# Kernel optimization log

Hardware: AMD Instinct MI355X
Metric: run time of the kernel (lower is better)

The kernel has to match this reference:

```python
import jax, jax.numpy as jnp
import numpy as np

NEG_MASK = -999.0  # matches masked_fill_(-999) in the torch source

def setup_inputs() -> dict:
    key = jax.random.key(0)
    ks = jax.random.split(key, 8)
    B, N, D = 4, 2048, 768      # batch, nodes, in_dim
    H, Do = 6, 128              # att_head, out_dim (D == H*Do)
    feat_in = jax.random.normal(ks[0], (B, N, D), dtype=jnp.float32)
    adj = jax.random.randint(ks[1], (B, N, N), 0, 2).astype(jnp.int32)
    W = jax.random.normal(ks[2], (H, D, Do), dtype=jnp.float32) * (1.0 / np.sqrt(D))
    b = jnp.zeros((Do,), dtype=jnp.float32)
    w_src = jax.random.normal(ks[3], (H, Do, 1), dtype=jnp.float32) * (1.0 / np.sqrt(Do))
    w_dst = jax.random.normal(ks[4], (H, Do, 1), dtype=jnp.float32) * (1.0 / np.sqrt(Do))
    H_w = jax.random.normal(ks[5], (D, D), dtype=jnp.float32) * (1.0 / np.sqrt(D))
    H_b = jnp.zeros((D,), dtype=jnp.float32)
    return {"feat_in": feat_in, "adj": adj, "W": W, "b": b,
            "w_src": w_src, "w_dst": w_dst, "H_w": H_w, "H_b": H_b}

def reference(feat_in, adj, W, b, w_src, w_dst, H_w, H_b):
    leaky_alpha = 0.2
    B, N, D = feat_in.shape
    Hh = W.shape[0]
    # per-head projection: [B, H, N, Do]
    h = jnp.einsum('bni,hio->bhno', feat_in, W)
    th = jnp.tanh(h)
    attn_src = jnp.einsum('bhno,hoz->bhnz', th, w_src)  # [B,H,N,1]
    attn_dst = jnp.einsum('bhno,hoz->bhnz', th, w_dst)  # [B,H,N,1]
    # additive scores: src_i + dst_j -> [B,H,N,N]
    attn = attn_src + jnp.swapaxes(attn_dst, -1, -2)
    attn = jnp.where(attn >= 0, attn, leaky_alpha * attn)
    mask = (adj == 0)[:, None, :, :]  # [B,1,N,N]
    attn = jnp.where(mask, NEG_MASK, attn)
    attn = jax.nn.softmax(attn, axis=-1)
    feat_out = jnp.einsum('bhnm,bhmo->bhno', attn, h) + b  # [B,H,N,Do]
    feat_out = jnp.swapaxes(feat_out, 1, 2).reshape(B, N, -1)  # [B,N,H*Do]
    feat_out = jax.nn.elu(feat_out)
    gate = jax.nn.sigmoid(feat_in @ H_w.T + H_b)
    out = gate * feat_out + (1.0 - gate) * feat_in
    return out
```

## Files before the change

### kernel.cpp

```cpp
#include <hip/hip_runtime.h>
#include <hip/hip_bf16.h>

#define B_ 4
#define N_ 2048
#define D_ 768
#define H_ 6
#define Do_ 128
#define M_ (B_*N_)
#define C2_ (2*D_)
#define SROW 49152

typedef __attribute__((ext_vector_type(8))) short bf16x8;
typedef __attribute__((ext_vector_type(4))) float f32x4;
typedef __attribute__((ext_vector_type(4))) int int4v;
typedef __attribute__((ext_vector_type(2))) int int2v;
typedef __attribute__((ext_vector_type(4))) float float4v;
typedef __attribute__((ext_vector_type(4))) unsigned short ushort4v;

__device__ __forceinline__ float b2f(short s){
    unsigned u = ((unsigned)(unsigned short)s) << 16;
    return __builtin_bit_cast(float, u);
}
__device__ __forceinline__ short f2b(float f){
    unsigned u = __builtin_bit_cast(unsigned, f);
    unsigned r = (u + 0x7fffu + ((u >> 16) & 1u)) >> 16;
    return (short)r;
}
__device__ __forceinline__ int pk2(float a, float b){
    unsigned ua = __builtin_bit_cast(unsigned, a) + 0x8000u;
    unsigned ub = __builtin_bit_cast(unsigned, b) + 0x8000u;
    return (int)__builtin_amdgcn_perm(ub, ua, 0x07060302u);
}
__device__ __forceinline__ float fast_tanh(float x){
    float a = fabsf(x);
    float e = __expf(-2.0f * a);
    float t = (1.0f - e) / (1.0f + e);
    return copysignf(t, x);
}

#define HT_IDX(bh, n, o) ((((size_t)((bh)*64 + ((n) >> 5))*128 + (o))*32) + ((n) & 31))

__global__ __launch_bounds__(256) void k_prep_pack(const float* __restrict__ W,
                                                   const float* __restrict__ Hw,
                                                   const int* __restrict__ adj,
                                                   short* __restrict__ bmat,
                                                   unsigned char* __restrict__ pk){
    int bid = blockIdx.x, t = threadIdx.x;
    if (bid < C2_){
        int c = bid;
        if (c < D_){
            int hd = c >> 7, o = c & 127;
            const float* wp = W + hd*D_*Do_ + o;
            for (int k = t; k < D_; k += 256) bmat[c*D_ + k] = f2b(wp[k*Do_]);
        } else {
            int d = c - D_;
            const float* hp = Hw + d*D_;
            for (int k = t; k < D_; k += 256) bmat[c*D_ + k] = f2b(hp[k]);
        }
    } else {
        int g = (bid - C2_)*256 + t;
        const int* ap = adj + (size_t)g*8;
        int4v a0 = *(const int4v*)ap;
        int4v a1 = *(const int4v*)(ap + 4);
        unsigned by = 0;
        #pragma unroll
        for (int i = 0; i < 4; i++){
            by |= (a0[i] ? 1u : 0u) << i;
            by |= (a1[i] ? 1u : 0u) << (i + 4);
        }
        pk[g] = (unsigned char)by;
    }
}

__global__ __launch_bounds__(256) void k_gemm(const float* __restrict__ A,
                                              const short* __restrict__ Bm,
                                              short* __restrict__ ht,
                                              float* outg){
    __shared__ short As[128][72];
    __shared__ short Bs[128][72];
    int tid = threadIdx.x;
    int mBase = blockIdx.y * 128, cBase = blockIdx.x * 128;
    int wave = tid >> 6, lane = tid & 63, q = lane >> 4, nL = lane & 15;
    int wr = (wave >> 1) * 64, wc = (wave & 1) * 64;
    f32x4 acc[4][4] = {};
    for (int kk = 0; kk < D_; kk += 64){
        __syncthreads();
        #pragma unroll
        for (int i = 0; i < 8; i++){
            int idx = tid + i*256;
            int row = idx >> 4, c4 = (idx & 15) * 4;
            float4v av = *(const float4v*)&A[(mBase+row)*D_ + kk + c4];
            int2v w; w[0] = pk2(av[0], av[1]); w[1] = pk2(av[2], av[3]);
            *(int2v*)&As[row][c4] = w;
        }
        #pragma unroll
        for (int i = 0; i < 4; i++){
            int idx = tid + i*256;
            int row = idx >> 3, cs = (idx & 7) * 8;
            *(int4v*)&Bs[row][cs] = *(const int4v*)&Bm[(cBase+row)*D_ + kk + cs];
        }
        __syncthreads();
        #pragma unroll
        for (int k2 = 0; k2 < 64; k2 += 32){
            bf16x8 aF[4], bF[4];
            #pragma unroll
            for (int rt = 0; rt < 4; rt++) aF[rt] = *(const bf16x8*)&As[wr + rt*16 + nL][k2 + q*8];
            #pragma unroll
            for (int ct = 0; ct < 4; ct++) bF[ct] = *(const bf16x8*)&Bs[wc + ct*16 + nL][k2 + q*8];
            #pragma unroll
            for (int rt = 0; rt < 4; rt++)
                #pragma unroll
                for (int ct = 0; ct < 4; ct++)
                    acc[rt][ct] = __builtin_amdgcn_mfma_f32_16x16x32_bf16(aF[rt], bF[ct], acc[rt][ct], 0, 0, 0);
        }
    }
    if (cBase < D_){
        int hd = cBase >> 7;
        #pragma unroll
        for (int rt = 0; rt < 4; rt++){
            #pragma unroll
            for (int ct = 0; ct < 4; ct++){
                int o  = (wc + ct*16 + nL) & 127;
                int m0 = mBase + wr + rt*16 + q*4;
                int b = m0 >> 11, n0 = m0 & 2047;
                int bh = b*H_ + hd;
                ushort4v v;
                #pragma unroll
                for (int r = 0; r < 4; r++) v[r] = (unsigned short)f2b(acc[rt][ct][r]);
                *(ushort4v*)&ht[HT_IDX(bh, n0, o)] = v;
            }
        }
    } else {
        #pragma unroll
        for (int rt = 0; rt < 4; rt++){
            #pragma unroll
            for (int ct = 0; ct < 4; ct++){
                int d  = cBase - D_ + wc + ct*16 + nL;
                int m0 = mBase + wr + rt*16 + q*4;
                #pragma unroll
                for (int r = 0; r < 4; r++) outg[(size_t)(m0 + r)*D_ + d] = acc[rt][ct][r];
            }
        }
    }
}

__global__ __launch_bounds__(256) void k_stats(const short* __restrict__ ht,
                                               const float* __restrict__ wsrc,
                                               const float* __restrict__ wdst,
                                               float* __restrict__ srcP,
                                               float* __restrict__ dstP){
    int g = blockIdx.x * 256 + threadIdx.x;
    int y = blockIdx.y, o0 = y * 32;
    int bh = g >> 11, n = g & 2047;
    int hd = bh % H_;
    const short* hp = ht + HT_IDX(bh, n, o0);
    const float* ws = wsrc + hd*Do_ + o0;
    const float* wd = wdst + hd*Do_ + o0;
    float as = 0.f, ad = 0.f;
    for (int o = 0; o < 32; o++){
        float t = fast_tanh(b2f(hp[o*32]));
        as += t * ws[o];
        ad += t * wd[o];
    }
    srcP[y*SROW + g] = as; dstP[y*SROW + g] = ad;
}

struct StageS {
    float E1[2048];
    float E2[2048];
    unsigned pkw[64*65];
};
struct RedS { float red[2][64][37]; };
union LdsU { StageS s; RedS r; };

#define PV_EPILOGUE(ACC, ACCL, FOFF)                                          \
    {                                                                         \
        _Pragma("unroll")                                                     \
        for (int r = 0; r < 4; r++){                                          \
            int i = r0 + rh*32 + (FOFF) + q*4 + r;                            \
            float invl = 1.0f / (ACCL)[r];                                    \
            size_t baseO = (size_t)(b*N_ + i)*D_ + hd*Do_;                    \
            _Pragma("unroll")                                                 \
            for (int ct = 0; ct < 8; ct++){                                   \
                int o = ct*16 + nL;                                           \
                float v = (ACC)[ct][r]*invl + bias[o];                        \
                float e = v > 0.f ? v : __expf(v) - 1.0f;                     \
                float gl = outg[baseO + o] + Hb[hd*Do_ + o];                  \
                float g = 1.0f / (1.0f + __expf(-gl));                        \
                float fi = feat_in[baseO + o];                                \
                outg[baseO + o] = g*e + (1.0f - g)*fi;                        \
            }                                                                 \
        }                                                                     \
    }

__global__ __launch_bounds__(256) void k_pv(const unsigned char* __restrict__ pkG,
                                            const float* __restrict__ srcP,
                                            const float* __restrict__ dstP,
                                            const short* __restrict__ ht,
                                            const float* __restrict__ feat_in,
                                            const float* __restrict__ bias,
                                            const float* __restrict__ Hb,
                                            float* outg){
    __shared__ LdsU U;
    int lid = blockIdx.x;
    int nid = (lid & 7)*96 + (lid >> 3);
    int itile = nid & 31;
    int hd = (nid >> 5) % 6, b = nid / 192;
    int tid = threadIdx.x, wave = tid >> 6, lane = tid & 63, q = lane >> 4, nL = lane & 15;
    int rh = wave >> 1, kh = wave & 1;
    int r0 = itile * 64;
    int bh = b*H_ + hd;
    {
        const float4v* g0 = (const float4v*)(dstP + bh*N_);
        const float4v* g1 = (const float4v*)(dstP + SROW + bh*N_);
        const float4v* g2 = (const float4v*)(dstP + 2*SROW + bh*N_);
        const float4v* g3 = (const float4v*)(dstP + 3*SROW + bh*N_);
        #pragma unroll
        for (int h = 0; h < 2; h++){
            int c4 = tid*2 + h;
            float4v d = g0[c4] + g1[c4] + g2[c4] + g3[c4];
            #pragma unroll
            for (int t = 0; t < 4; t++){
                U.s.E1[c4*4 + t] = __expf(d[t]);
                U.s.E2[c4*4 + t] = __expf(0.2f * d[t]);
            }
        }
        const unsigned* pg = (const unsigned*)(pkG + (size_t)(b*N_ + r0) * (N_/8));
        #pragma unroll
        for (int k = 0; k < 16; k++){
            int idx = tid + k*256;
            U.s.pkw[(idx >> 6)*65 + (idx & 63)] = pg[idx];
        }
    }
    __syncthreads();
    int rowL0 = rh*32 + nL, rowL1 = rowL0 + 16;
    int gi0 = bh*N_ + r0 + rowL0, gi1 = bh*N_ + r0 + rowL1;
    float s0 = srcP[gi0] + srcP[SROW+gi0] + srcP[2*SROW+gi0] + srcP[3*SROW+gi0];
    float s1 = srcP[gi1] + srcP[SROW+gi1] + srcP[2*SROW+gi1] + srcP[3*SROW+gi1];
    float e1r0 = __expf(s0), e2r0 = __expf(0.2f*s0);
    float e1r1 = __expf(s1), e2r1 = __expf(0.2f*s1);
    bf16x8 vone;
    #pragma unroll
    for (int t = 0; t < 8; t++) vone[t] = (short)0x3F80;
    const short* hp = ht + (size_t)bh*262144;
    f32x4 acc[2][8] = {};
    f32x4 accl0 = {}, accl1 = {};
    int base0 = rowL0*65, base1 = rowL1*65;
    int jEnd = kh*1024 + 1024;
    for (int j0 = kh*1024; j0 < jEnd; j0 += 32){
        unsigned by0 = (U.s.pkw[base0 + (j0 >> 5)] >> (q*8)) & 0xFF;
        unsigned by1 = (U.s.pkw[base1 + (j0 >> 5)] >> (q*8)) & 0xFF;
        int kb = j0 + q*8;
        const short* hj = hp + (size_t)(j0 >> 5)*4096 + q*8;
        float4v E1a = *(const float4v*)&U.s.E1[kb];
        float4v E1b = *(const float4v*)&U.s.E1[kb + 4];
        float4v E2a = *(const float4v*)&U.s.E2[kb];
        float4v E2b = *(const float4v*)&U.s.E2[kb + 4];
        float p0[8], p1[8];
        #pragma unroll
        for (int t = 0; t < 8; t++){
            float E1t = t < 4 ? E1a[t] : E1b[t-4];
            float E2t = t < 4 ? E2a[t] : E2b[t-4];
            float a0 = fmaxf(e1r0*E1t, e2r0*E2t);
            float a1 = fmaxf(e1r1*E1t, e2r1*E2t);
            p0[t] = ((by0 >> t) & 1u) ? a0 : 0.0f;
            p1[t] = ((by1 >> t) & 1u) ? a1 : 0.0f;
        }
        int4v pi0, pi1;
        #pragma unroll
        for (int tp = 0; tp < 4; tp++){
            pi0[tp] = pk2(p0[2*tp], p0[2*tp+1]);
            pi1[tp] = pk2(p1[2*tp], p1[2*tp+1]);
        }
        bf16x8 pf0 = __builtin_bit_cast(bf16x8, pi0);
        bf16x8 pf1 = __builtin_bit_cast(bf16x8, pi1);
        #pragma unroll
        for (int ct = 0; ct < 8; ct++){
            bf16x8 bF = *(const bf16x8*)&hj[(ct*16 + nL)*32];
            acc[0][ct] = __builtin_amdgcn_mfma_f32_16x16x32_bf16(pf0, bF, acc[0][ct], 0, 0, 0);
            acc[1][ct] = __builtin_amdgcn_mfma_f32_16x16x32_bf16(pf1, bF, acc[1][ct], 0, 0, 0);
        }
        accl0 = __builtin_amdgcn_mfma_f32_16x16x32_bf16(pf0, vone, accl0, 0, 0, 0);
        accl1 = __builtin_amdgcn_mfma_f32_16x16x32_bf16(pf1, vone, accl1, 0, 0, 0);
    }
    __syncthreads();
    if (kh == 1){
        #pragma unroll
        for (int ct = 0; ct < 8; ct++)
            #pragma unroll
            for (int r = 0; r < 4; r++) U.r.red[rh][lane][ct*4 + r] = acc[0][ct][r];
        #pragma unroll
        for (int r = 0; r < 4; r++) U.r.red[rh][lane][32 + r] = accl0[r];
    }
    __syncthreads();
    if (kh == 0){
        #pragma unroll
        for (int ct = 0; ct < 8; ct++)
            #pragma unroll
            for (int r = 0; r < 4; r++) acc[0][ct][r] += U.r.red[rh][lane][ct*4 + r];
        #pragma unroll
        for (int r = 0; r < 4; r++) accl0[r] += U.r.red[rh][lane][32 + r];
    }
    __syncthreads();
    if (kh == 0){
        #pragma unroll
        for (int ct = 0; ct < 8; ct++)
            #pragma unroll
            for (int r = 0; r < 4; r++) U.r.red[rh][lane][ct*4 + r] = acc[1][ct][r];
        #pragma unroll
        for (int r = 0; r < 4; r++) U.r.red[rh][lane][32 + r] = accl1[r];
    }
    __syncthreads();
    if (kh == 1){
        #pragma unroll
        for (int ct = 0; ct < 8; ct++)
            #pragma unroll
            for (int r = 0; r < 4; r++) acc[1][ct][r] += U.r.red[rh][lane][ct*4 + r];
        #pragma unroll
        for (int r = 0; r < 4; r++) accl1[r] += U.r.red[rh][lane][32 + r];
    }
    if (kh == 0){
        PV_EPILOGUE(acc[0], accl0, 0)
    } else {
        PV_EPILOGUE(acc[1], accl1, 16)
    }
}

extern "C" void kernel_launch(void* const* d_in, const int* in_sizes, int n_in,
                              void* d_out, int out_size, void* d_ws, size_t ws_size,
                              hipStream_t stream){
    const float* feat = (const float*)d_in[0];
    const int*   adj  = (const int*)  d_in[1];
    const float* W    = (const float*)d_in[2];
    const float* bias = (const float*)d_in[3];
    const float* wsrc = (const float*)d_in[4];
    const float* wdst = (const float*)d_in[5];
    const float* Hw   = (const float*)d_in[6];
    const float* Hb   = (const float*)d_in[7];
    float* out = (float*)d_out;
    char* ws = (char*)d_ws;
    short* bmat = (short*)(ws);
    short* ht   = (short*)(ws + 2359296);
    float* srcP = (float*)(ws + 14942208);
    float* dstP = (float*)(ws + 15728640);
    unsigned char* pk = (unsigned char*)(ws + 16515072);

    hipLaunchKernelGGL(k_prep_pack, dim3(C2_ + 8192), dim3(256), 0, stream, W, Hw, adj, bmat, pk);
    hipLaunchKernelGGL(k_gemm,      dim3(12, 64),     dim3(256), 0, stream, feat, bmat, ht, out);
    hipLaunchKernelGGL(k_stats,     dim3(192, 4),     dim3(256), 0, stream, ht, wsrc, wdst, srcP, dstP);
    hipLaunchKernelGGL(k_pv,        dim3(768),        dim3(256), 0, stream, pk, srcP, dstP,
                       ht, feat, bias, Hb, out);
}
```

Baseline: 269.7 us.

## Transpose W via LDS tiles and load GEMM B operand with global_load_lds

The prep kernel now transposes W in 128x128 LDS tiles with coalesced float4 reads and 16-byte writes, replacing strided per-column gathers. The GEMM loads its bf16 B tile straight from global memory into LDS with global_load_lds, using an XOR-swizzled unpadded layout to avoid bank conflicts, which removes the register round-trip. The direct-to-LDS load depends on the lane-to-address mapping matching the swizzled layout, and both the prep and GEMM kernels are a small share of total time.

```diff
diff --git a/kernel.cpp b/kernel.cpp
--- a/kernel.cpp
+++ b/kernel.cpp
@@ -37,6 +37,11 @@
     float t = (1.0f - e) / (1.0f + e);
     return copysignf(t, x);
 }
+__device__ __forceinline__ void gload_lds16(const void* g, void* l){
+    __builtin_amdgcn_global_load_lds((const __attribute__((address_space(1))) unsigned int*)g,
+                                     (__attribute__((address_space(3))) unsigned int*)l,
+                                     16, 0, 0);
+}
 
 #define HT_IDX(bh, n, o) ((((size_t)((bh)*64 + ((n) >> 5))*128 + (o))*32) + ((n) & 31))
 
@@ -45,20 +50,32 @@
                                                    const int* __restrict__ adj,
                                                    short* __restrict__ bmat,
                                                    unsigned char* __restrict__ pk){
+    __shared__ short Ts[128][136];
     int bid = blockIdx.x, t = threadIdx.x;
-    if (bid < C2_){
-        int c = bid;
-        if (c < D_){
-            int hd = c >> 7, o = c & 127;
-            const float* wp = W + hd*D_*Do_ + o;
-            for (int k = t; k < D_; k += 256) bmat[c*D_ + k] = f2b(wp[k*Do_]);
-        } else {
-            int d = c - D_;
-            const float* hp = Hw + d*D_;
-            for (int k = t; k < D_; k += 256) bmat[c*D_ + k] = f2b(hp[k]);
-        }
+    if (bid < 36){
+        int hd = bid / 6, kc = bid % 6, k0 = kc * 128;
+        const float* wb = W + (size_t)hd*D_*Do_ + (size_t)k0*Do_;
+        #pragma unroll
+        for (int i = 0; i < 16; i++){
+            int u = t + i*256;
+            int krow = u >> 5, o4 = (u & 31) * 4;
+            float4v v = *(const float4v*)&wb[krow*Do_ + o4];
+            #pragma unroll
+            for (int e = 0; e < 4; e++) Ts[o4 + e][krow] = f2b(v[e]);
+        }
+        __syncthreads();
+        #pragma unroll
+        for (int i = 0; i < 8; i++){
+            int u = t + i*256;
+            int orow = u >> 4, cu = (u & 15) * 8;
+            *(int4v*)&bmat[(size_t)(hd*128 + orow)*D_ + k0 + cu] = *(const int4v*)&Ts[orow][cu];
+        }
+    } else if (bid < 36 + D_){
+        int d = bid - 36;
+        const float* hp = Hw + (size_t)d*D_;
+        for (int k = t; k < D_; k += 256) bmat[(size_t)(D_ + d)*D_ + k] = f2b(hp[k]);
     } else {
-        int g = (bid - C2_)*256 + t;
+        int g = (bid - 36 - D_)*256 + t;
         const int* ap = adj + (size_t)g*8;
         int4v a0 = *(const int4v*)ap;
         int4v a1 = *(const int4v*)(ap + 4);
@@ -77,14 +94,21 @@
                                               short* __restrict__ ht,
                                               float* outg){
     __shared__ short As[128][72];
-    __shared__ short Bs[128][72];
+    __shared__ short Bs[128*64];
     int tid = threadIdx.x;
     int mBase = blockIdx.y * 128, cBase = blockIdx.x * 128;
     int wave = tid >> 6, lane = tid & 63, q = lane >> 4, nL = lane & 15;
     int wr = (wave >> 1) * 64, wc = (wave & 1) * 64;
+    int srow = tid >> 3;
+    int sc16 = (tid & 7) ^ (srow & 7);
+    const short* bSrc = Bm + (size_t)(cBase + srow)*D_ + sc16*8;
+    short* bDst = &Bs[wave*512];
     f32x4 acc[4][4] = {};
     for (int kk = 0; kk < D_; kk += 64){
         __syncthreads();
+        #pragma unroll
+        for (int i = 0; i < 4; i++)
+            gload_lds16(bSrc + (size_t)i*32*D_ + kk, bDst + i*2048);
         #pragma unroll
         for (int i = 0; i < 8; i++){
             int idx = tid + i*256;
@@ -93,20 +117,18 @@
             int2v w; w[0] = pk2(av[0], av[1]); w[1] = pk2(av[2], av[3]);
             *(int2v*)&As[row][c4] = w;
         }
-        #pragma unroll
-        for (int i = 0; i < 4; i++){
-            int idx = tid + i*256;
-            int row = idx >> 3, cs = (idx & 7) * 8;
-            *(int4v*)&Bs[row][cs] = *(const int4v*)&Bm[(cBase+row)*D_ + kk + cs];
-        }
         __syncthreads();
         #pragma unroll
         for (int k2 = 0; k2 < 64; k2 += 32){
             bf16x8 aF[4], bF[4];
+            int cb = (k2 >> 3) + q;
             #pragma unroll
             for (int rt = 0; rt < 4; rt++) aF[rt] = *(const bf16x8*)&As[wr + rt*16 + nL][k2 + q*8];
             #pragma unroll
-            for (int ct = 0; ct < 4; ct++) bF[ct] = *(const bf16x8*)&Bs[wc + ct*16 + nL][k2 + q*8];
+            for (int ct = 0; ct < 4; ct++){
+                int r = wc + ct*16 + nL;
+                bF[ct] = *(const bf16x8*)&Bs[r*64 + ((cb ^ (r & 7)) * 8)];
+            }
             #pragma unroll
             for (int rt = 0; rt < 4; rt++)
                 #pragma unroll
@@ -345,7 +367,7 @@
     float* dstP = (float*)(ws + 15728640);
     unsigned char* pk = (unsigned char*)(ws + 16515072);
 
-    hipLaunchKernelGGL(k_prep_pack, dim3(C2_ + 8192), dim3(256), 0, stream, W, Hw, adj, bmat, pk);
+    hipLaunchKernelGGL(k_prep_pack, dim3(36 + D_ + 8192), dim3(256), 0, stream, W, Hw, adj, bmat, pk);
     hipLaunchKernelGGL(k_gemm,      dim3(12, 64),     dim3(256), 0, stream, feat, bmat, ht, out);
     hipLaunchKernelGGL(k_stats,     dim3(192, 4),     dim3(256), 0, stream, ht, wsrc, wdst, srcP, dstP);
     hipLaunchKernelGGL(k_pv,        dim3(768),        dim3(256), 0, stream, pk, srcP, dstP,
```

After: 268.8 us. No clear change (-0.3%).
